# Performance work log

Hardware: AMD Instinct MI355X
Metric: run time of the kernel (lower is better)

Reference implementation:

```python
import jax, jax.numpy as jnp
import numpy as np


def setup_inputs() -> dict:
    key = jax.random.key(0)
    k1, k2 = jax.random.split(key)
    N, C, H, W = 2, 128, 256, 256
    k, m = 7, 8
    feat = jax.random.normal(k1, (N, C, H, W), dtype=jnp.float32)
    filters_lr = jax.random.normal(k2, (N, C * k * k, H // m, W // m), dtype=jnp.float32)
    return {"feat": feat, "filters_lr": filters_lr, "kernel_size": k, "block_size": m}


def _block_fac(feat, filters_lr, k, m):
    # feat: [N,C,H,W]; filters_lr: [N, C*k^2, H/m, W/m]
    N, C, H, W = feat.shape
    Hb, Wb = H // m, W // m
    k2 = k * k
    pad = (k - 1) // 2
    # weight_permute_reshape: NCHW -> NHWC -> [N,Hb,Wb,C,k2] (C slowest, then tap)
    w = jnp.transpose(filters_lr, (0, 2, 3, 1)).reshape(N, Hb, Wb, C, k2)
    x = jnp.transpose(feat, (0, 2, 3, 1))  # NHWC
    xp = jnp.pad(x, ((0, 0), (pad, pad), (pad, pad), (0, 0)))
    out = jnp.zeros_like(x)
    # tap index t = dh*k + dw (matches torch unfold(2,k) then unfold(3,k) ordering)
    for t in range(k2):
        dh, dw = t // k, t % k
        # per-block weight for this tap, upsampled to full resolution: [N,H,W,C]
        w_t = jnp.repeat(jnp.repeat(w[..., t], m, axis=1), m, axis=2)
        out = out + xp[:, dh:dh + H, dw:dw + W, :] * w_t
    return jnp.transpose(out, (0, 3, 1, 2))  # back to NCHW


def reference(feat, filters_lr, kernel_size, block_size):
    return _block_fac(feat, filters_lr, kernel_size, block_size)
```

## Files before the change

kernel.cpp:

```cpp
#include <hip/hip_runtime.h>
#include <stdint.h>


#define LDW   264
#define NROWS 38

typedef const uint32_t __attribute__((address_space(1))) guint;
typedef uint32_t __attribute__((address_space(3))) luint;

__global__ __launch_bounds__(256, 1)
void block_fac_kernel(const float* __restrict__ feat,
                      const float* __restrict__ filt,
                      float* __restrict__ out) {
    __shared__ float s_in[NROWS * LDW];

    const int bid = blockIdx.x;
    const int hb4 = bid & 7;
    const int c   = (bid >> 3) & 127;
    const int n   = bid >> 10;
    const int tid = threadIdx.x;

    const int lane = tid & 63;
    const int wave = tid >> 6;
    const int c0   = lane << 2;
    const int wb   = lane >> 1;
    const int r0   = wave << 3;
    const int hb   = hb4 * 4 + wave;

    const float* wgbase = filt + (size_t)((n * 128 + c) * 49) * 1024 + hb * 32 + wb;
    float wt[49];
    #pragma unroll
    for (int t = 0; t < 49; ++t) wt[t] = wgbase[(size_t)t * 1024];

    const int H0 = hb4 * 32;
    const int h0 = H0 - 3;

    if (tid < NROWS * 6) {
        int r = tid / 6, j = tid - r * 6;
        int p = (j < 3) ? (1 + j) : (257 + j);
        s_in[r * LDW + p] = 0.f;
    }

    const float* fbase = feat + (size_t)(n * 128 + c) * (256 * 256);
    for (int idx = tid; idx < NROWS * 64; idx += 256) {
        int r  = idx >> 6;
        int gr = h0 + r;
        float* lp = &s_in[r * LDW + 4];
        if (gr >= 0 && gr < 256) {
            const float* gp = fbase + (size_t)gr * 256 + ((idx & 63) << 2);
            __builtin_amdgcn_global_load_lds((guint*)gp, (luint*)lp, 16, 0, 0);
        } else {
            *(float4*)(&s_in[r * LDW + 4 + ((idx & 63) << 2)]) =
                make_float4(0.f, 0.f, 0.f, 0.f);
        }
    }
    __syncthreads();

    float acc[8][4] = {};

    #pragma unroll
    for (int jj = 0; jj < 14; ++jj) {
        const float* rp = &s_in[(r0 + jj) * LDW + c0];
        float4 a0 = *(const float4*)(rp);
        float4 a1 = *(const float4*)(rp + 4);
        float4 a2 = *(const float4*)(rp + 8);
        float win[12] = {a0.x, a0.y, a0.z, a0.w,
                         a1.x, a1.y, a1.z, a1.w,
                         a2.x, a2.y, a2.z, a2.w};
        #pragma unroll
        for (int a = 0; a < 8; ++a) {
            int dh = jj - a;
            if (dh >= 0 && dh <= 6) {
                #pragma unroll
                for (int dw = 0; dw < 7; ++dw) {
                    float wv = wt[dh * 7 + dw];
                    #pragma unroll
                    for (int i = 0; i < 4; ++i)
                        acc[a][i] += win[i + dw + 1] * wv;
                }
            }
        }
    }

    float* obase = out + (size_t)((n * 128 + c) * 256 + H0 + r0) * 256 + c0;
    #pragma unroll
    for (int a = 0; a < 8; ++a)
        *(float4*)(obase + (size_t)(a * 256)) =
            make_float4(acc[a][0], acc[a][1], acc[a][2], acc[a][3]);
}

extern "C" void kernel_launch(void* const* d_in, const int* in_sizes, int n_in,
                              void* d_out, int out_size, void* d_ws, size_t ws_size,
                              hipStream_t stream) {
    const float* feat = (const float*)d_in[0];
    const float* filt = (const float*)d_in[1];
    float* out = (float*)d_out;
    dim3 grid(2 * 128 * 8);
    dim3 block(256);
    hipLaunchKernelGGL(block_fac_kernel, grid, block, 0, stream, feat, filt, out);
}
```

Baseline: 42.97 us.

## Split work into single-wave blocks per 8-row band and drop block barrier

Each block shrinks from four waves sharing a 38-row LDS tile to one wave that loads its own 14-row halo tile and computes one 8-row block band. The grid grows 4x. Because a block is now a single wave, the __syncthreads is replaced with an s_waitcnt vmcnt(0) on the async global-to-LDS loads. This removes barrier stalls and gives finer-grained scheduling, but raises redundant halo reads of the feature map from about 38/32 to 14/8 per output row.

```diff
diff --git a/kernel.cpp b/kernel.cpp
--- a/kernel.cpp
+++ b/kernel.cpp
@@ -3,64 +3,60 @@
 
 
 #define LDW   264
-#define NROWS 38
+#define NROWS 14
 
 typedef const uint32_t __attribute__((address_space(1))) guint;
 typedef uint32_t __attribute__((address_space(3))) luint;
 
-__global__ __launch_bounds__(256, 1)
+__global__ __launch_bounds__(64, 2)
 void block_fac_kernel(const float* __restrict__ feat,
                       const float* __restrict__ filt,
                       float* __restrict__ out) {
     __shared__ float s_in[NROWS * LDW];
 
     const int bid = blockIdx.x;
-    const int hb4 = bid & 7;
-    const int c   = (bid >> 3) & 127;
-    const int n   = bid >> 10;
-    const int tid = threadIdx.x;
+    const int hb  = bid & 31;
+    const int c   = (bid >> 5) & 127;
+    const int n   = bid >> 12;
+    const int lane = threadIdx.x;
 
-    const int lane = tid & 63;
-    const int wave = tid >> 6;
-    const int c0   = lane << 2;
-    const int wb   = lane >> 1;
-    const int r0   = wave << 3;
-    const int hb   = hb4 * 4 + wave;
+    const int c0 = lane << 2;
+    const int wb = lane >> 1;
 
     const float* wgbase = filt + (size_t)((n * 128 + c) * 49) * 1024 + hb * 32 + wb;
     float wt[49];
     #pragma unroll
     for (int t = 0; t < 49; ++t) wt[t] = wgbase[(size_t)t * 1024];
 
-    const int H0 = hb4 * 32;
+    const int H0 = hb * 8;
     const int h0 = H0 - 3;
 
-    if (tid < NROWS * 6) {
-        int r = tid / 6, j = tid - r * 6;
+    for (int idx = lane; idx < NROWS * 6; idx += 64) {
+        int r = idx / 6, j = idx - r * 6;
         int p = (j < 3) ? (1 + j) : (257 + j);
         s_in[r * LDW + p] = 0.f;
     }
 
     const float* fbase = feat + (size_t)(n * 128 + c) * (256 * 256);
-    for (int idx = tid; idx < NROWS * 64; idx += 256) {
-        int r  = idx >> 6;
+    #pragma unroll
+    for (int r = 0; r < NROWS; ++r) {
         int gr = h0 + r;
         float* lp = &s_in[r * LDW + 4];
         if (gr >= 0 && gr < 256) {
-            const float* gp = fbase + (size_t)gr * 256 + ((idx & 63) << 2);
+            const float* gp = fbase + (size_t)gr * 256 + (lane << 2);
             __builtin_amdgcn_global_load_lds((guint*)gp, (luint*)lp, 16, 0, 0);
         } else {
-            *(float4*)(&s_in[r * LDW + 4 + ((idx & 63) << 2)]) =
+            *(float4*)(&s_in[r * LDW + 4 + (lane << 2)]) =
                 make_float4(0.f, 0.f, 0.f, 0.f);
         }
     }
-    __syncthreads();
+    asm volatile("s_waitcnt vmcnt(0)" ::: "memory");
 
     float acc[8][4] = {};
 
     #pragma unroll
-    for (int jj = 0; jj < 14; ++jj) {
-        const float* rp = &s_in[(r0 + jj) * LDW + c0];
+    for (int jj = 0; jj < NROWS; ++jj) {
+        const float* rp = &s_in[jj * LDW + c0];
         float4 a0 = *(const float4*)(rp);
         float4 a1 = *(const float4*)(rp + 4);
         float4 a2 = *(const float4*)(rp + 8);
@@ -82,7 +78,7 @@
         }
     }
 
-    float* obase = out + (size_t)((n * 128 + c) * 256 + H0 + r0) * 256 + c0;
+    float* obase = out + (size_t)((n * 128 + c) * 256 + H0) * 256 + c0;
     #pragma unroll
     for (int a = 0; a < 8; ++a)
         *(float4*)(obase + (size_t)(a * 256)) =
@@ -95,7 +91,7 @@
     const float* feat = (const float*)d_in[0];
     const float* filt = (const float*)d_in[1];
     float* out = (float*)d_out;
-    dim3 grid(2 * 128 * 8);
-    dim3 block(256);
+    dim3 grid(2 * 128 * 32);
+    dim3 block(64);
     hipLaunchKernelGGL(block_fac_kernel, grid, block, 0, stream, feat, filt, out);
 }
```

New measurement: 43.62 us. About the same (+1.5%).
